# Kernel tuning notes

Hardware: AMD Instinct MI355X
Metric: run time of the kernel (lower is better)

Reference implementation:

```python
import jax, jax.numpy as jnp
import numpy as np

NEG_INF = -1e30
D_MODEL = 128


def setup_inputs() -> dict:
    key = jax.random.key(0)
    k1, k2, k3 = jax.random.split(key, 3)
    B, D, Lc, Lq = 64, D_MODEL, 1024, 256
    C = jax.random.normal(k1, (B, D, Lc), dtype=jnp.float32)
    Q = jax.random.normal(k2, (B, D, Lq), dtype=jnp.float32)
    cmask = jnp.ones((B, Lc), dtype=jnp.float32)
    qmask = jnp.ones((B, Lq), dtype=jnp.float32)
    lim = (1.0 / D) ** 0.5
    w = jax.random.uniform(k3, (3 * D,), dtype=jnp.float32, minval=-lim, maxval=lim)
    return {"C": C, "Q": Q, "cmask": cmask, "qmask": qmask, "w": w}


def reference(C, Q, cmask, qmask, w):
    # C: (B, D, Lc), Q: (B, D, Lq), w: (3D,)
    D = C.shape[1]
    Ct = jnp.swapaxes(C, 1, 2)  # (B, Lc, D)
    Qt = jnp.swapaxes(Q, 1, 2)  # (B, Lq, D)
    w1, w2, w3 = w[:D], w[D:2 * D], w[2 * D:]
    # Decomposed trilinear similarity: equivalent to cat([Ct,Qt,Ct*Qt]) @ w
    S = (jnp.einsum('bld,d->bl', Ct, w1)[:, :, None]
         + jnp.einsum('bmd,d->bm', Qt, w2)[:, None, :]
         + jnp.einsum('bld,bmd->blm', Ct * w3, Qt))  # (B, Lc, Lq)
    qm = qmask[:, None, :]  # (B, 1, Lq)
    cm = cmask[:, :, None]  # (B, Lc, 1)
    S1 = jax.nn.softmax(S + (1.0 - qm) * NEG_INF, axis=2)
    S2 = jax.nn.softmax(S + (1.0 - cm) * NEG_INF, axis=1)
    A = jnp.einsum('blm,bmd->bld', S1, Qt)  # (B, Lc, D)
    S12 = jnp.einsum('blm,bnm->bln', S1, S2)  # (B, Lc, Lc)
    Bv = jnp.einsum('bln,bnd->bld', S12, Ct)  # (B, Lc, D)
    out = jnp.concatenate([Ct, A, Ct * A, Ct * Bv], axis=2)  # (B, Lc, 4D)
    # dropout is identity in eval mode
    return jnp.swapaxes(out, 1, 2)  # (B, 4D, Lc)
```

## Files before the change

### kernel.cpp

```cpp
#include <hip/hip_runtime.h>

#define NB  64
#define ND  128
#define NLC 1024
#define NLQ 256
#define FNEG (-1e30f)

typedef __bf16 bf16x8 __attribute__((ext_vector_type(8)));
typedef float f32x4 __attribute__((ext_vector_type(4)));

__device__ __forceinline__ ushort f2bf(float x) {
  unsigned u = __float_as_uint(x);
  return (ushort)((u + 0x7fffu + ((u >> 16) & 1u)) >> 16);
}
__device__ __forceinline__ float bf2f(ushort u) {
  return __uint_as_float((unsigned)u << 16);
}
__device__ __forceinline__ bf16x8 ldfrag(const ushort* p) {
  return *reinterpret_cast<const bf16x8*>(p);
}
__device__ __forceinline__ uint4 pack8(float a0, float a1, float a2, float a3,
                                       float a4, float a5, float a6, float a7) {
  uint4 pk;
  pk.x = (unsigned)f2bf(a0) | ((unsigned)f2bf(a1) << 16);
  pk.y = (unsigned)f2bf(a2) | ((unsigned)f2bf(a3) << 16);
  pk.z = (unsigned)f2bf(a4) | ((unsigned)f2bf(a5) << 16);
  pk.w = (unsigned)f2bf(a6) | ((unsigned)f2bf(a7) << 16);
  return pk;
}

__global__ __launch_bounds__(256) void convert_kernel(
    const float* __restrict__ C, const float* __restrict__ Q,
    const float* __restrict__ w,
    ushort* __restrict__ Ctw3, ushort* __restrict__ Qt16,
    ushort* __restrict__ Cn16, ushort* __restrict__ Qn16,
    float* __restrict__ c1part, float* __restrict__ q2part,
    float* __restrict__ out) {
  __shared__ float tile[64][65];
  __shared__ float cred[64][4];
  int b = blockIdx.y;
  int tid = blockIdx.x;
  int t = threadIdx.x, c = t & 63, r0 = t >> 6;
  if (tid < 32) {
    int d0 = (tid >> 4) * 64, l0 = (tid & 15) * 64;
    const float* src = C + (size_t)b * ND * NLC;
    float* o0 = out + (size_t)b * 4 * ND * NLC;
    float part = 0.f;
#pragma unroll
    for (int p = 0; p < 16; ++p) {
      int r = r0 + p * 4;
      float v = src[(size_t)(d0 + r) * NLC + l0 + c];
      tile[c][r] = v * w[2 * ND + d0 + r];
      part += v * w[d0 + r];
      o0[(size_t)(d0 + r) * NLC + l0 + c] = v;
    }
    cred[c][r0] = part;
    __syncthreads();
    ushort* dst = Ctw3 + (size_t)b * NLC * ND;
#pragma unroll
    for (int p = 0; p < 16; ++p) {
      int r = r0 + p * 4;
      dst[(size_t)(l0 + r) * ND + d0 + c] = f2bf(tile[r][c]);
    }
    if (t < 64)
      c1part[(size_t)(tid >> 4) * NB * NLC + b * NLC + l0 + t] =
          cred[t][0] + cred[t][1] + cred[t][2] + cred[t][3];
  } else if (tid < 40) {
    int q = tid - 32;
    int d0 = (q >> 2) * 64, m0 = (q & 3) * 64;
    const float* src = Q + (size_t)b * ND * NLQ;
    float part = 0.f;
#pragma unroll
    for (int p = 0; p < 16; ++p) {
      int r = r0 + p * 4;
      float v = src[(size_t)(d0 + r) * NLQ + m0 + c];
      tile[c][r] = v;
      part += v * w[ND + d0 + r];
    }
    cred[c][r0] = part;
    __syncthreads();
    ushort* dst = Qt16 + (size_t)b * NLQ * ND;
#pragma unroll
    for (int p = 0; p < 16; ++p) {
      int r = r0 + p * 4;
      dst[(size_t)(m0 + r) * ND + d0 + c] = f2bf(tile[r][c]);
    }
    if (t < 64)
      q2part[(size_t)(q >> 2) * NB * NLQ + b * NLQ + m0 + t] =
          cred[t][0] + cred[t][1] + cred[t][2] + cred[t][3];
  } else if (tid < 56) {
    size_t ofs = (size_t)(tid - 40) * 8192;
    const float* src = C + (size_t)b * ND * NLC + ofs;
    ushort* dst = Cn16 + (size_t)b * ND * NLC + ofs;
#pragma unroll
    for (int it = 0; it < 4; ++it) {
      int e = (it * 256 + t) * 8;
      float4 v0 = *(const float4*)(src + e), v1 = *(const float4*)(src + e + 4);
      *(uint4*)(dst + e) = pack8(v0.x, v0.y, v0.z, v0.w, v1.x, v1.y, v1.z, v1.w);
    }
  } else {
    size_t ofs = (size_t)(tid - 56) * 16384;
    const float* src = Q + (size_t)b * ND * NLQ + ofs;
    ushort* dst = Qn16 + (size_t)b * ND * NLQ + ofs;
#pragma unroll
    for (int it = 0; it < 8; ++it) {
      int e = (it * 256 + t) * 8;
      float4 v0 = *(const float4*)(src + e), v1 = *(const float4*)(src + e + 4);
      *(uint4*)(dst + e) = pack8(v0.x, v0.y, v0.z, v0.w, v1.x, v1.y, v1.z, v1.w);
    }
  }
}

__global__ __launch_bounds__(512, 4) void score_stats(
    const ushort* __restrict__ Ctw3, const ushort* __restrict__ Qt16,
    const float* __restrict__ c1part, const float* __restrict__ q2part,
    const float* __restrict__ cmask, const float* __restrict__ qmask,
    ushort* __restrict__ e1g, ushort* __restrict__ e1t,
    float* __restrict__ rscale_g, float* __restrict__ psum_part,
    float* __restrict__ chunkmax_g) {
  __shared__ union {
    struct { __align__(16) ushort As[128 * 32]; __align__(16) ushort Bs[256 * 32]; } s;
    struct { float rowred[128][4]; float rowsum[128][4]; float colred[256][2]; } red;
    __align__(16) ushort bounce[128 * 264];
    __align__(16) ushort bounce2[256 * 136];
  } u;
  __shared__ float rmaxs[128];
  __shared__ float rcs[128];
  __shared__ float cnegs[128];
  __shared__ float qnegs[256];
  __shared__ float c1s[128];
  __shared__ float q2s[256];
  __shared__ float chunkmax_s;

  int b = blockIdx.y, chunk = blockIdx.x, l0 = chunk * 128;
  int t = threadIdx.x, lane = t & 63, wid = t >> 6;
  int wy = wid >> 2, wx = wid & 3, ln = lane & 15, qd = lane >> 4;

  if (t < 128) {
    int idx = b * NLC + l0 + t;
    c1s[t] = c1part[idx] + c1part[NB * NLC + idx];
    cnegs[t] = (1.f - cmask[idx]) * FNEG;
  } else if (t < 384) {
    int m = t - 128;
    int idx = b * NLQ + m;
    q2s[m] = q2part[idx] + q2part[NB * NLQ + idx];
    qnegs[m] = (1.f - qmask[idx]) * FNEG;
  }

  const ushort* Ab = Ctw3 + (size_t)b * NLC * ND;
  const ushort* Bb = Qt16 + (size_t)b * NLQ * ND;
  f32x4 acc[4][4];
#pragma unroll
  for (int i = 0; i < 4; ++i)
#pragma unroll
    for (int j = 0; j < 4; ++j) acc[i][j] = (f32x4){0.f, 0.f, 0.f, 0.f};

  for (int kk = 0; kk < ND; kk += 32) {
#pragma unroll
    for (int p = 0; p < 3; ++p) {
      int e4 = p * 512 + t;
      if (e4 < 512) {
        int r = e4 >> 2, cc = (e4 & 3) * 8;
        *(int4*)(u.s.As + r * 32 + cc) = *(const int4*)(Ab + (size_t)(l0 + r) * ND + kk + cc);
      } else {
        int e = e4 - 512;
        int r = e >> 2, cc = (e & 3) * 8;
        *(int4*)(u.s.Bs + r * 32 + cc) = *(const int4*)(Bb + (size_t)r * ND + kk + cc);
      }
    }
    __syncthreads();
    bf16x8 af[4], bfr[4];
#pragma unroll
    for (int i = 0; i < 4; ++i) {
      af[i]  = ldfrag(u.s.As + (wy * 64 + i * 16 + ln) * 32 + qd * 8);
      bfr[i] = ldfrag(u.s.Bs + (wx * 64 + i * 16 + ln) * 32 + qd * 8);
    }
#pragma unroll
    for (int i = 0; i < 4; ++i)
#pragma unroll
      for (int j = 0; j < 4; ++j)
        acc[i][j] = __builtin_amdgcn_mfma_f32_16x16x32_bf16(af[i], bfr[j], acc[i][j], 0, 0, 0);
    __syncthreads();
  }

  float qnj[4], q2j[4];
#pragma unroll
  for (int j = 0; j < 4; ++j) {
    int m = wx * 64 + j * 16 + ln;
    qnj[j] = qnegs[m];
    q2j[j] = q2s[m];
  }
#pragma unroll
  for (int i = 0; i < 4; ++i)
#pragma unroll
    for (int r = 0; r < 4; ++r) {
      int ll = wy * 64 + i * 16 + qd * 4 + r;
      float cv = c1s[ll];
#pragma unroll
      for (int j = 0; j < 4; ++j) acc[i][j][r] += cv + q2j[j];
    }

#pragma unroll
  for (int i = 0; i < 4; ++i)
#pragma unroll
    for (int r = 0; r < 4; ++r) {
      float v = -INFINITY;
#pragma unroll
      for (int j = 0; j < 4; ++j) v = fmaxf(v, acc[i][j][r] + qnj[j]);
      v = fmaxf(v, __shfl_xor(v, 1));
      v = fmaxf(v, __shfl_xor(v, 2));
      v = fmaxf(v, __shfl_xor(v, 4));
      v = fmaxf(v, __shfl_xor(v, 8));
      if (ln == 0) u.red.rowred[wy * 64 + i * 16 + qd * 4 + r][wx] = v;
    }
  __syncthreads();
  if (t < 128) {
    float v = fmaxf(fmaxf(u.red.rowred[t][0], u.red.rowred[t][1]),
                    fmaxf(u.red.rowred[t][2], u.red.rowred[t][3]));
    rmaxs[t] = v;
    rcs[t] = v + cnegs[t];
  }
  __syncthreads();
  if (t < 64) {
    float v = fmaxf(rcs[t], rcs[t + 64]);
    v = fmaxf(v, __shfl_xor(v, 1));
    v = fmaxf(v, __shfl_xor(v, 2));
    v = fmaxf(v, __shfl_xor(v, 4));
    v = fmaxf(v, __shfl_xor(v, 8));
    v = fmaxf(v, __shfl_xor(v, 16));
    v = fmaxf(v, __shfl_xor(v, 32));
    if (t == 0) chunkmax_s = v;
  }
  __syncthreads();
  if (t < 128) rcs[t] = __expf(rcs[t] - chunkmax_s);
  __syncthreads();

  float cs[4] = {0.f, 0.f, 0.f, 0.f};
#pragma unroll
  for (int i = 0; i < 4; ++i)
#pragma unroll
    for (int r = 0; r < 4; ++r) {
      int ll = wy * 64 + i * 16 + qd * 4 + r;
      float rmx = rmaxs[ll], rf = rcs[ll];
      float rs = 0.f;
#pragma unroll
      for (int j = 0; j < 4; ++j) {
        float e = __expf(acc[i][j][r] + qnj[j] - rmx);
        acc[i][j][r] = e;
        rs += e;
        cs[j] += e * rf;
      }
      rs += __shfl_xor(rs, 1);
      rs += __shfl_xor(rs, 2);
      rs += __shfl_xor(rs, 4);
      rs += __shfl_xor(rs, 8);
      if (ln == 0) u.red.rowsum[ll][wx] = rs;
    }
#pragma unroll
  for (int j = 0; j < 4; ++j) {
    float v = cs[j];
    v += __shfl_xor(v, 16);
    v += __shfl_xor(v, 32);
    if (qd == 0) u.red.colred[wx * 64 + j * 16 + ln][wy] = v;
  }
  __syncthreads();
  if (t < 128)
    rscale_g[b * NLC + l0 + t] = 1.f / (u.red.rowsum[t][0] + u.red.rowsum[t][1] +
                                        u.red.rowsum[t][2] + u.red.rowsum[t][3]);
  if (t >= 256 && t < 512) {
    int m = t - 256;
    psum_part[(b * 8 + chunk) * NLQ + m] = u.red.colred[m][0] + u.red.colred[m][1];
  }
  if (t == 0) chunkmax_g[b * 8 + chunk] = chunkmax_s;
  __syncthreads();

#pragma unroll
  for (int i = 0; i < 4; ++i)
#pragma unroll
    for (int r = 0; r < 4; ++r) {
      int ll = wy * 64 + i * 16 + qd * 4 + r;
#pragma unroll
      for (int j = 0; j < 4; ++j)
        u.bounce[ll * 264 + wx * 64 + j * 16 + ln] = f2bf(acc[i][j][r]);
    }
  __syncthreads();
  ushort* Eb = e1g + (size_t)b * NLC * NLQ;
#pragma unroll
  for (int p = 0; p < 8; ++p) {
    int idx4 = p * 512 + t;
    int r = idx4 >> 5, c = (idx4 & 31) * 8;
    *(int4*)(Eb + (size_t)(l0 + r) * NLQ + c) = *(const int4*)(u.bounce + r * 264 + c);
  }
  __syncthreads();

#pragma unroll
  for (int i = 0; i < 4; ++i)
#pragma unroll
    for (int r = 0; r < 4; ++r) {
      int ll = wy * 64 + i * 16 + qd * 4 + r;
      float rf = rcs[ll];
#pragma unroll
      for (int j = 0; j < 4; ++j)
        u.bounce2[(wx * 64 + j * 16 + ln) * 136 + ll] = f2bf(acc[i][j][r] * rf);
    }
  __syncthreads();
  ushort* Etb = e1t + (size_t)b * NLQ * NLC;
#pragma unroll
  for (int p = 0; p < 8; ++p) {
    int idx4 = p * 512 + t;
    int m = idx4 >> 4, l8 = idx4 & 15;
    *(int4*)(Etb + (size_t)m * NLC + l0 + l8 * 8) =
        *(const int4*)(u.bounce2 + m * 136 + l8 * 8);
  }
}

__global__ __launch_bounds__(256) void stat_combine(
    const float* __restrict__ psum_part, const float* __restrict__ chunkmax_g,
    float* __restrict__ cinv) {
  __shared__ float cm[8];
  int b = blockIdx.x, t = threadIdx.x;
  if (t < 8) cm[t] = chunkmax_g[b * 8 + t];
  __syncthreads();
  float K = cm[0];
#pragma unroll
  for (int c = 1; c < 8; ++c) K = fmaxf(K, cm[c]);
  float s = 0.f;
#pragma unroll
  for (int c = 0; c < 8; ++c)
    s += psum_part[(b * 8 + c) * NLQ + t] * __expf(cm[c] - K);
  cinv[b * NLQ + t] = 1.f / s;
}

__global__ __launch_bounds__(512) void tmat_mfma(
    const ushort* __restrict__ Cn16, const ushort* __restrict__ e1t,
    const float* __restrict__ chunkmax_g, ushort* __restrict__ Tpart) {
  __shared__ __align__(16) ushort As[128 * 32];
  __shared__ __align__(16) ushort Bs[256 * 32];
  int b = blockIdx.y, ks = blockIdx.x;
  int t = threadIdx.x, lane = t & 63, wid = t >> 6;
  int wy = wid >> 2, wx = wid & 3, ln = lane & 15, qd = lane >> 4;
  const ushort* Cb = Cn16 + (size_t)b * ND * NLC;
  const ushort* Eb = e1t + (size_t)b * NLQ * NLC;
  float cm0 = chunkmax_g[b * 8 + 2 * ks];
  float cm1 = chunkmax_g[b * 8 + 2 * ks + 1];
  int first = (cm0 <= cm1) ? 0 : 1;
  float resc = __expf(fminf(cm0, cm1) - fmaxf(cm0, cm1));
  f32x4 acc[4][4];
#pragma unroll
  for (int i = 0; i < 4; ++i)
#pragma unroll
    for (int j = 0; j < 4; ++j) acc[i][j] = (f32x4){0.f, 0.f, 0.f, 0.f};

  for (int h = 0; h < 2; ++h) {
    int lbase = (2 * ks + (h ? 1 - first : first)) * 128;
    for (int c0 = 0; c0 < 128; c0 += 32) {
#pragma unroll
      for (int p = 0; p < 3; ++p) {
        int e4 = p * 512 + t;
        if (e4 < 512) {
          int r = e4 >> 2, cc = (e4 & 3) * 8;
          *(int4*)(As + r * 32 + cc) =
              *(const int4*)(Cb + (size_t)r * NLC + lbase + c0 + cc);
        } else {
          int e = e4 - 512;
          int rm = e >> 2, cc = (e & 3) * 8;
          *(int4*)(Bs + rm * 32 + cc) =
              *(const int4*)(Eb + (size_t)rm * NLC + lbase + c0 + cc);
        }
      }
      __syncthreads();
      bf16x8 af[4], bfr[4];
#pragma unroll
      for (int i = 0; i < 4; ++i) {
        af[i]  = ldfrag(As + (wy * 64 + i * 16 + ln) * 32 + qd * 8);
        bfr[i] = ldfrag(Bs + (wx * 64 + i * 16 + ln) * 32 + qd * 8);
      }
#pragma unroll
      for (int i = 0; i < 4; ++i)
#pragma unroll
        for (int j = 0; j < 4; ++j)
          acc[i][j] = __builtin_amdgcn_mfma_f32_16x16x32_bf16(af[i], bfr[j], acc[i][j], 0, 0, 0);
      __syncthreads();
    }
    if (h == 0) {
#pragma unroll
      for (int i = 0; i < 4; ++i)
#pragma unroll
        for (int j = 0; j < 4; ++j)
#pragma unroll
          for (int r = 0; r < 4; ++r) acc[i][j][r] *= resc;
    }
  }
  ushort* Tb = Tpart + ((size_t)(b * 4 + ks)) * ND * NLQ;
#pragma unroll
  for (int i = 0; i < 4; ++i)
#pragma unroll
    for (int r = 0; r < 4; ++r) {
      int d = wy * 64 + i * 16 + qd * 4 + r;
#pragma unroll
      for (int j = 0; j < 4; ++j) {
        int m = wx * 64 + j * 16 + ln;
        Tb[(size_t)d * NLQ + m] = f2bf(acc[i][j][r]);
      }
    }
}

__global__ __launch_bounds__(256) void tcombine(
    const ushort* __restrict__ Tpart, const float* __restrict__ cinv,
    const float* __restrict__ chunkmax_g, ushort* __restrict__ Tt) {
  int gid = blockIdx.x * 256 + threadIdx.x;
  int e = gid * 8;
  int b = e >> 15;
  int r = e & 32767;
  int m = r & 255;
  const float* cmb = chunkmax_g + b * 8;
  float K = cmb[0];
#pragma unroll
  for (int c = 1; c < 8; ++c) K = fmaxf(K, cmb[c]);
  float s[8] = {0.f, 0.f, 0.f, 0.f, 0.f, 0.f, 0.f, 0.f};
#pragma unroll
  for (int ks = 0; ks < 4; ++ks) {
    float fac = __expf(fmaxf(cmb[2 * ks], cmb[2 * ks + 1]) - K);
    int4 v = *(const int4*)(Tpart + ((size_t)(b * 4 + ks)) * ND * NLQ + r);
    const ushort* sv = (const ushort*)&v;
#pragma unroll
    for (int k = 0; k < 8; ++k) s[k] += fac * bf2f(sv[k]);
  }
  float4 ci0 = *(const float4*)(cinv + b * NLQ + m);
  float4 ci1 = *(const float4*)(cinv + b * NLQ + m + 4);
  *(uint4*)(Tt + (size_t)b * ND * NLQ + r) =
      pack8(s[0] * ci0.x, s[1] * ci0.y, s[2] * ci0.z, s[3] * ci0.w,
            s[4] * ci1.x, s[5] * ci1.y, s[6] * ci1.z, s[7] * ci1.w);
}

__global__ __launch_bounds__(512, 4) void outk(
    const float* __restrict__ C, const ushort* __restrict__ Qn16,
    const ushort* __restrict__ Tt, const ushort* __restrict__ e1g,
    const float* __restrict__ rscale, float* __restrict__ out) {
  __shared__ union {
    struct { __align__(16) ushort As1[128 * 32]; __align__(16) ushort As2[128 * 32];
             __align__(16) ushort Bs[128 * 32]; } st;
    struct { float a[32][132]; float bv[32][132]; } ep;
  } u;
  int b = blockIdx.y;
  int l0 = blockIdx.x * 128;
  const ushort* Qb = Qn16 + (size_t)b * ND * NLQ;
  const ushort* Tb = Tt + (size_t)b * ND * NLQ;
  const ushort* Eb = e1g + (size_t)b * NLC * NLQ;
  int t = threadIdx.x, lane = t & 63, wid = t >> 6;
  int wy = wid >> 2, wx = wid & 3;
  int ln = lane & 15, qd = lane >> 4;
  f32x4 acc1[4][2], acc2[4][2];
#pragma unroll
  for (int i = 0; i < 4; ++i)
#pragma unroll
    for (int j = 0; j < 2; ++j) {
      acc1[i][j] = (f32x4){0.f, 0.f, 0.f, 0.f};
      acc2[i][j] = (f32x4){0.f, 0.f, 0.f, 0.f};
    }

  for (int m0 = 0; m0 < NLQ; m0 += 32) {
    {
      int r = t >> 2, cc = (t & 3) * 8;
      *(int4*)(u.st.As1 + r * 32 + cc) = *(const int4*)(Qb + (size_t)r * NLQ + m0 + cc);
      *(int4*)(u.st.As2 + r * 32 + cc) = *(const int4*)(Tb + (size_t)r * NLQ + m0 + cc);
      *(int4*)(u.st.Bs + r * 32 + cc)  = *(const int4*)(Eb + (size_t)(l0 + r) * NLQ + m0 + cc);
    }
    __syncthreads();
    bf16x8 a1[4], a2[4], bfr[2];
#pragma unroll
    for (int i = 0; i < 4; ++i) {
      a1[i] = ldfrag(u.st.As1 + (wy * 64 + i * 16 + ln) * 32 + qd * 8);
      a2[i] = ldfrag(u.st.As2 + (wy * 64 + i * 16 + ln) * 32 + qd * 8);
    }
#pragma unroll
    for (int j = 0; j < 2; ++j)
      bfr[j] = ldfrag(u.st.Bs + (wx * 32 + j * 16 + ln) * 32 + qd * 8);
#pragma unroll
    for (int i = 0; i < 4; ++i)
#pragma unroll
      for (int j = 0; j < 2; ++j) {
        acc1[i][j] = __builtin_amdgcn_mfma_f32_16x16x32_bf16(a1[i], bfr[j], acc1[i][j], 0, 0, 0);
        acc2[i][j] = __builtin_amdgcn_mfma_f32_16x16x32_bf16(a2[i], bfr[j], acc2[i][j], 0, 0, 0);
      }
    __syncthreads();
  }

  float rsj[2];
#pragma unroll
  for (int j = 0; j < 2; ++j)
    rsj[j] = rscale[b * NLC + l0 + wx * 32 + j * 16 + ln];

  const float* Cbase = C + (size_t)b * ND * NLC;
  float* outb = out + (size_t)b * 4 * ND * NLC;
#pragma unroll
  for (int db = 0; db < 4; ++db) {
    __syncthreads();
    if (wy == (db >> 1)) {
      int ibase = (db & 1) * 2;
#pragma unroll
      for (int ii = 0; ii < 2; ++ii) {
        int i = ibase + ii;
#pragma unroll
        for (int j = 0; j < 2; ++j) {
          int lc = wx * 32 + j * 16 + ln;
#pragma unroll
          for (int r = 0; r < 4; ++r) {
            int dr = ii * 16 + qd * 4 + r;
            u.ep.a[dr][lc]  = acc1[i][j][r] * rsj[j];
            u.ep.bv[dr][lc] = acc2[i][j][r] * rsj[j];
          }
        }
      }
    }
    __syncthreads();
    int row = t >> 4, colf = (t & 15) * 8;
    int d = db * 32 + row;
    const float* Crow = Cbase + (size_t)d * NLC + l0 + colf;
    float4 c0 = *(const float4*)(Crow), c1 = *(const float4*)(Crow + 4);
    float4 a0 = *(const float4*)&u.ep.a[row][colf];
    float4 a1v = *(const float4*)&u.ep.a[row][colf + 4];
    float4 b0 = *(const float4*)&u.ep.bv[row][colf];
    float4 b1 = *(const float4*)&u.ep.bv[row][colf + 4];
    float* oA = outb + (size_t)(128 + d) * NLC + l0 + colf;
    float* oCA = outb + (size_t)(256 + d) * NLC + l0 + colf;
    float* oCB = outb + (size_t)(384 + d) * NLC + l0 + colf;
    *(float4*)(oA) = a0;
    *(float4*)(oA + 4) = a1v;
    *(float4*)(oCA) = (float4){c0.x * a0.x, c0.y * a0.y, c0.z * a0.z, c0.w * a0.w};
    *(float4*)(oCA + 4) = (float4){c1.x * a1v.x, c1.y * a1v.y, c1.z * a1v.z, c1.w * a1v.w};
    *(float4*)(oCB) = (float4){c0.x * b0.x, c0.y * b0.y, c0.z * b0.z, c0.w * b0.w};
    *(float4*)(oCB + 4) = (float4){c1.x * b1.x, c1.y * b1.y, c1.z * b1.z, c1.w * b1.w};
  }
}

extern "C" void kernel_launch(void* const* d_in, const int* in_sizes, int n_in,
                              void* d_out, int out_size, void* d_ws, size_t ws_size,
                              hipStream_t stream) {
  const float* C     = (const float*)d_in[0];
  const float* Q     = (const float*)d_in[1];
  const float* cmask = (const float*)d_in[2];
  const float* qmask = (const float*)d_in[3];
  const float* w     = (const float*)d_in[4];
  float* out = (float*)d_out;

  char* p = (char*)d_ws;
  auto alloc = [&](size_t bytes) { char* r = p; p += (bytes + 255) & ~(size_t)255; return r; };
  ushort* e1g    = (ushort*)alloc((size_t)NB * NLC * NLQ * 2);
  ushort* e1t    = (ushort*)alloc((size_t)NB * NLQ * NLC * 2);
  ushort* Ctw3   = (ushort*)alloc((size_t)NB * NLC * ND * 2);
  ushort* Qt16   = (ushort*)alloc((size_t)NB * NLQ * ND * 2);
  ushort* Cn16   = (ushort*)alloc((size_t)NB * ND * NLC * 2);
  ushort* Qn16   = (ushort*)alloc((size_t)NB * ND * NLQ * 2);
  ushort* Tpart  = (ushort*)alloc((size_t)NB * 4 * ND * NLQ * 2);
  ushort* Tt     = (ushort*)alloc((size_t)NB * ND * NLQ * 2);
  float*  c1part = (float*)alloc((size_t)2 * NB * NLC * 4);
  float*  q2part = (float*)alloc((size_t)2 * NB * NLQ * 4);
  float*  rscale = (float*)alloc((size_t)NB * NLC * 4);
  float*  cinv   = (float*)alloc((size_t)NB * NLQ * 4);
  float*  psum   = (float*)alloc((size_t)NB * 8 * NLQ * 4);
  float*  chmax  = (float*)alloc((size_t)NB * 8 * 4);

  convert_kernel<<<dim3(58, NB), 256, 0, stream>>>(C, Q, w, Ctw3, Qt16, Cn16, Qn16,
                                                   c1part, q2part, out);
  score_stats<<<dim3(NLC / 128, NB), 512, 0, stream>>>(
      Ctw3, Qt16, c1part, q2part, cmask, qmask, e1g, e1t, rscale, psum, chmax);
  stat_combine<<<NB, 256, 0, stream>>>(psum, chmax, cinv);
  tmat_mfma<<<dim3(4, NB), 512, 0, stream>>>(Cn16, e1t, chmax, Tpart);
  tcombine<<<(NB * ND * NLQ / 8) / 256, 256, 0, stream>>>(Tpart, cinv, chmax, Tt);
  outk<<<dim3(NLC / 128, NB), 512, 0, stream>>>(C, Qn16, Tt, e1g, rscale, out);
}
```

Measured before the change: 265.4 us.

## Fuse bf16 casts into transpose blocks, fold row scale into E1, split tmat blocks

```diff
diff --git a/kernel.cpp b/kernel.cpp
--- a/kernel.cpp
+++ b/kernel.cpp
@@ -45,14 +45,17 @@
     int d0 = (tid >> 4) * 64, l0 = (tid & 15) * 64;
     const float* src = C + (size_t)b * ND * NLC;
     float* o0 = out + (size_t)b * 4 * ND * NLC;
+    ushort* cn = Cn16 + (size_t)b * ND * NLC;
     float part = 0.f;
 #pragma unroll
     for (int p = 0; p < 16; ++p) {
       int r = r0 + p * 4;
-      float v = src[(size_t)(d0 + r) * NLC + l0 + c];
+      size_t idx = (size_t)(d0 + r) * NLC + l0 + c;
+      float v = src[idx];
       tile[c][r] = v * w[2 * ND + d0 + r];
       part += v * w[d0 + r];
-      o0[(size_t)(d0 + r) * NLC + l0 + c] = v;
+      o0[idx] = v;
+      cn[idx] = f2bf(v);
     }
     cred[c][r0] = part;
     __syncthreads();
@@ -65,17 +68,20 @@
     if (t < 64)
       c1part[(size_t)(tid >> 4) * NB * NLC + b * NLC + l0 + t] =
           cred[t][0] + cred[t][1] + cred[t][2] + cred[t][3];
-  } else if (tid < 40) {
+  } else {
     int q = tid - 32;
     int d0 = (q >> 2) * 64, m0 = (q & 3) * 64;
     const float* src = Q + (size_t)b * ND * NLQ;
+    ushort* qn = Qn16 + (size_t)b * ND * NLQ;
     float part = 0.f;
 #pragma unroll
     for (int p = 0; p < 16; ++p) {
       int r = r0 + p * 4;
-      float v = src[(size_t)(d0 + r) * NLQ + m0 + c];
+      size_t idx = (size_t)(d0 + r) * NLQ + m0 + c;
+      float v = src[idx];
       tile[c][r] = v;
       part += v * w[ND + d0 + r];
+      qn[idx] = f2bf(v);
     }
     cred[c][r0] = part;
     __syncthreads();
@@ -88,26 +94,6 @@
     if (t < 64)
       q2part[(size_t)(q >> 2) * NB * NLQ + b * NLQ + m0 + t] =
           cred[t][0] + cred[t][1] + cred[t][2] + cred[t][3];
-  } else if (tid < 56) {
-    size_t ofs = (size_t)(tid - 40) * 8192;
-    const float* src = C + (size_t)b * ND * NLC + ofs;
-    ushort* dst = Cn16 + (size_t)b * ND * NLC + ofs;
-#pragma unroll
-    for (int it = 0; it < 4; ++it) {
-      int e = (it * 256 + t) * 8;
-      float4 v0 = *(const float4*)(src + e), v1 = *(const float4*)(src + e + 4);
-      *(uint4*)(dst + e) = pack8(v0.x, v0.y, v0.z, v0.w, v1.x, v1.y, v1.z, v1.w);
-    }
-  } else {
-    size_t ofs = (size_t)(tid - 56) * 16384;
-    const float* src = Q + (size_t)b * ND * NLQ + ofs;
-    ushort* dst = Qn16 + (size_t)b * ND * NLQ + ofs;
-#pragma unroll
-    for (int it = 0; it < 8; ++it) {
-      int e = (it * 256 + t) * 8;
-      float4 v0 = *(const float4*)(src + e), v1 = *(const float4*)(src + e + 4);
-      *(uint4*)(dst + e) = pack8(v0.x, v0.y, v0.z, v0.w, v1.x, v1.y, v1.z, v1.w);
-    }
   }
 }
 
@@ -116,8 +102,7 @@
     const float* __restrict__ c1part, const float* __restrict__ q2part,
     const float* __restrict__ cmask, const float* __restrict__ qmask,
     ushort* __restrict__ e1g, ushort* __restrict__ e1t,
-    float* __restrict__ rscale_g, float* __restrict__ psum_part,
-    float* __restrict__ chunkmax_g) {
+    float* __restrict__ psum_part, float* __restrict__ chunkmax_g) {
   __shared__ union {
     struct { __align__(16) ushort As[128 * 32]; __align__(16) ushort Bs[256 * 32]; } s;
     struct { float rowred[128][4]; float rowsum[128][4]; float colred[256][2]; } red;
@@ -126,6 +111,7 @@
   } u;
   __shared__ float rmaxs[128];
   __shared__ float rcs[128];
+  __shared__ float rss[128];
   __shared__ float cnegs[128];
   __shared__ float qnegs[256];
   __shared__ float c1s[128];
@@ -265,8 +251,8 @@
   }
   __syncthreads();
   if (t < 128)
-    rscale_g[b * NLC + l0 + t] = 1.f / (u.red.rowsum[t][0] + u.red.rowsum[t][1] +
-                                        u.red.rowsum[t][2] + u.red.rowsum[t][3]);
+    rss[t] = 1.f / (u.red.rowsum[t][0] + u.red.rowsum[t][1] +
+                    u.red.rowsum[t][2] + u.red.rowsum[t][3]);
   if (t >= 256 && t < 512) {
     int m = t - 256;
     psum_part[(b * 8 + chunk) * NLQ + m] = u.red.colred[m][0] + u.red.colred[m][1];
@@ -279,9 +265,10 @@
 #pragma unroll
     for (int r = 0; r < 4; ++r) {
       int ll = wy * 64 + i * 16 + qd * 4 + r;
+      float rs = rss[ll];
 #pragma unroll
       for (int j = 0; j < 4; ++j)
-        u.bounce[ll * 264 + wx * 64 + j * 16 + ln] = f2bf(acc[i][j][r]);
+        u.bounce[ll * 264 + wx * 64 + j * 16 + ln] = f2bf(acc[i][j][r] * rs);
     }
   __syncthreads();
   ushort* Eb = e1g + (size_t)b * NLC * NLQ;
@@ -331,16 +318,16 @@
   cinv[b * NLQ + t] = 1.f / s;
 }
 
-__global__ __launch_bounds__(512) void tmat_mfma(
+__global__ __launch_bounds__(256, 2) void tmat_mfma(
     const ushort* __restrict__ Cn16, const ushort* __restrict__ e1t,
     const float* __restrict__ chunkmax_g, ushort* __restrict__ Tpart) {
   __shared__ __align__(16) ushort As[128 * 32];
-  __shared__ __align__(16) ushort Bs[256 * 32];
-  int b = blockIdx.y, ks = blockIdx.x;
+  __shared__ __align__(16) ushort Bs[128 * 32];
+  int b = blockIdx.y, ksm = blockIdx.x, ks = ksm >> 1, mh = ksm & 1;
   int t = threadIdx.x, lane = t & 63, wid = t >> 6;
-  int wy = wid >> 2, wx = wid & 3, ln = lane & 15, qd = lane >> 4;
+  int wy = wid >> 1, wx = wid & 1, ln = lane & 15, qd = lane >> 4;
   const ushort* Cb = Cn16 + (size_t)b * ND * NLC;
-  const ushort* Eb = e1t + (size_t)b * NLQ * NLC;
+  const ushort* Eb = e1t + (size_t)b * NLQ * NLC + (size_t)(mh * 128) * NLC;
   float cm0 = chunkmax_g[b * 8 + 2 * ks];
   float cm1 = chunkmax_g[b * 8 + 2 * ks + 1];
   int first = (cm0 <= cm1) ? 0 : 1;
@@ -355,18 +342,13 @@
     int lbase = (2 * ks + (h ? 1 - first : first)) * 128;
     for (int c0 = 0; c0 < 128; c0 += 32) {
 #pragma unroll
-      for (int p = 0; p < 3; ++p) {
-        int e4 = p * 512 + t;
-        if (e4 < 512) {
-          int r = e4 >> 2, cc = (e4 & 3) * 8;
-          *(int4*)(As + r * 32 + cc) =
-              *(const int4*)(Cb + (size_t)r * NLC + lbase + c0 + cc);
-        } else {
-          int e = e4 - 512;
-          int rm = e >> 2, cc = (e & 3) * 8;
-          *(int4*)(Bs + rm * 32 + cc) =
-              *(const int4*)(Eb + (size_t)rm * NLC + lbase + c0 + cc);
-        }
+      for (int p = 0; p < 2; ++p) {
+        int e4 = p * 256 + t;
+        int r = e4 >> 2, cc = (e4 & 3) * 8;
+        *(int4*)(As + r * 32 + cc) =
+            *(const int4*)(Cb + (size_t)r * NLC + lbase + c0 + cc);
+        *(int4*)(Bs + r * 32 + cc) =
+            *(const int4*)(Eb + (size_t)r * NLC + lbase + c0 + cc);
       }
       __syncthreads();
       bf16x8 af[4], bfr[4];
@@ -399,7 +381,7 @@
       int d = wy * 64 + i * 16 + qd * 4 + r;
 #pragma unroll
       for (int j = 0; j < 4; ++j) {
-        int m = wx * 64 + j * 16 + ln;
+        int m = mh * 128 + wx * 64 + j * 16 + ln;
         Tb[(size_t)d * NLQ + m] = f2bf(acc[i][j][r]);
       }
     }
@@ -436,7 +418,7 @@
 __global__ __launch_bounds__(512, 4) void outk(
     const float* __restrict__ C, const ushort* __restrict__ Qn16,
     const ushort* __restrict__ Tt, const ushort* __restrict__ e1g,
-    const float* __restrict__ rscale, float* __restrict__ out) {
+    float* __restrict__ out) {
   __shared__ union {
     struct { __align__(16) ushort As1[128 * 32]; __align__(16) ushort As2[128 * 32];
              __align__(16) ushort Bs[128 * 32]; } st;
@@ -486,11 +468,6 @@
     __syncthreads();
   }
 
-  float rsj[2];
-#pragma unroll
-  for (int j = 0; j < 2; ++j)
-    rsj[j] = rscale[b * NLC + l0 + wx * 32 + j * 16 + ln];
-
   const float* Cbase = C + (size_t)b * ND * NLC;
   float* outb = out + (size_t)b * 4 * ND * NLC;
 #pragma unroll
@@ -507,8 +484,8 @@
 #pragma unroll
           for (int r = 0; r < 4; ++r) {
             int dr = ii * 16 + qd * 4 + r;
-            u.ep.a[dr][lc]  = acc1[i][j][r] * rsj[j];
-            u.ep.bv[dr][lc] = acc2[i][j][r] * rsj[j];
+            u.ep.a[dr][lc]  = acc1[i][j][r];
+            u.ep.bv[dr][lc] = acc2[i][j][r];
           }
         }
       }
@@ -556,17 +533,16 @@
   ushort* Tt     = (ushort*)alloc((size_t)NB * ND * NLQ * 2);
   float*  c1part = (float*)alloc((size_t)2 * NB * NLC * 4);
   float*  q2part = (float*)alloc((size_t)2 * NB * NLQ * 4);
-  float*  rscale = (float*)alloc((size_t)NB * NLC * 4);
   float*  cinv   = (float*)alloc((size_t)NB * NLQ * 4);
   float*  psum   = (float*)alloc((size_t)NB * 8 * NLQ * 4);
   float*  chmax  = (float*)alloc((size_t)NB * 8 * 4);
 
-  convert_kernel<<<dim3(58, NB), 256, 0, stream>>>(C, Q, w, Ctw3, Qt16, Cn16, Qn16,
+  convert_kernel<<<dim3(40, NB), 256, 0, stream>>>(C, Q, w, Ctw3, Qt16, Cn16, Qn16,
                                                    c1part, q2part, out);
   score_stats<<<dim3(NLC / 128, NB), 512, 0, stream>>>(
-      Ctw3, Qt16, c1part, q2part, cmask, qmask, e1g, e1t, rscale, psum, chmax);
+      Ctw3, Qt16, c1part, q2part, cmask, qmask, e1g, e1t, psum, chmax);
   stat_combine<<<NB, 256, 0, stream>>>(psum, chmax, cinv);
-  tmat_mfma<<<dim3(4, NB), 512, 0, stream>>>(Cn16, e1t, chmax, Tpart);
+  tmat_mfma<<<dim3(8, NB), 256, 0, stream>>>(Cn16, e1t, chmax, Tpart);
   tcombine<<<(NB * ND * NLQ / 8) / 256, 256, 0, stream>>>(Tpart, cinv, chmax, Tt);
-  outk<<<dim3(NLC / 128, NB), 512, 0, stream>>>(C, Qn16, Tt, e1g, rscale, out);
-}
+  outk<<<dim3(NLC / 128, NB), 512, 0, stream>>>(C, Qn16, Tt, e1g, out);
+}
```

Measured after the change: 275.7 us. +3.9%, slower.
